# Optimization experiments

Measured on AMD Instinct MI355X. Metric: run time of the kernel, lower is better.

Reference implementation:

```python
import jax, jax.numpy as jnp
import numpy as np

DIM = 1024
N_HEADS = 16
HEAD_DIM = DIM // N_HEADS
BATCH = 2
SEQ = 2048


def rotate_half(x):
    x1, x2 = jnp.split(x, 2, axis=-1)
    return jnp.concatenate((-x2, x1), axis=-1)


def rope_cos_sin(seq_len, head_dim, dtype=jnp.float32):
    inv_freq = 1.0 / (10000.0 ** (jnp.arange(0, head_dim, 2, dtype=jnp.float32) / head_dim))
    t = jnp.arange(seq_len, dtype=jnp.float32)
    freqs = jnp.einsum('i,j->ij', t, inv_freq)          # [S, hd/2]
    emb = jnp.concatenate((freqs, freqs), axis=-1)       # [S, hd]
    return emb.astype(dtype)[None, :, None, :]           # [1, S, 1, hd] (cos/sin applied below)


def setup_inputs() -> dict:
    key = jax.random.key(0)
    k_x, k_q, k_k, k_v, k_o = jax.random.split(key, 5)
    scale = 1.0 / np.sqrt(DIM)
    x = jax.random.normal(k_x, (BATCH, SEQ, DIM), dtype=jnp.float32)
    Wq = jax.random.normal(k_q, (DIM, DIM), dtype=jnp.float32) * scale
    Wk = jax.random.normal(k_k, (DIM, DIM), dtype=jnp.float32) * scale
    Wv = jax.random.normal(k_v, (DIM, DIM), dtype=jnp.float32) * scale
    Wo = jax.random.normal(k_o, (DIM, DIM), dtype=jnp.float32) * scale
    # causal mask: scores masked where mask == 0
    mask = jnp.tril(jnp.ones((SEQ, SEQ), dtype=jnp.int32))[None, None, :, :]
    return {"x": x, "Wq": Wq, "Wk": Wk, "Wv": Wv, "Wo": Wo, "mask": mask}


def reference(x, Wq, Wk, Wv, Wo, mask):
    B, S, _ = x.shape
    # torch nn.Linear: y = x @ W.T
    q = (x @ Wq.T).reshape(B, S, N_HEADS, HEAD_DIM)
    k = (x @ Wk.T).reshape(B, S, N_HEADS, HEAD_DIM)
    v = (x @ Wv.T).reshape(B, S, N_HEADS, HEAD_DIM)
    ang = rope_cos_sin(S, HEAD_DIM, x.dtype)
    cos, sin = jnp.cos(ang), jnp.sin(ang)
    q = q * cos + rotate_half(q) * sin
    k = k * cos + rotate_half(k) * sin
    # [B, H, S, hd]
    q = q.transpose(0, 2, 1, 3)
    k = k.transpose(0, 2, 1, 3)
    v = v.transpose(0, 2, 1, 3)
    scores = jnp.einsum('bhqd,bhkd->bhqk', q, k) / np.sqrt(HEAD_DIM)
    scores = jnp.where(mask == 0, jnp.asarray(-1e9, scores.dtype), scores)
    attn = jax.nn.softmax(scores, axis=-1)
    out = jnp.einsum('bhqk,bhkd->bhqd', attn, v)
    out = out.transpose(0, 2, 1, 3).reshape(B, S, DIM)
    return out @ Wo.T
```

## Files before the change

### kernel.cpp

```cpp
#include <hip/hip_runtime.h>
#include <stdint.h>

typedef unsigned short u16;
typedef __bf16 bf16x8 __attribute__((ext_vector_type(8)));
typedef __bf16 bf16x4 __attribute__((ext_vector_type(4)));
typedef float f32x4 __attribute__((ext_vector_type(4)));

#define N_B 2
#define N_S 2048
#define N_D 1024
#define N_H 16
#define HD 64

#if __has_builtin(__builtin_amdgcn_exp2f)
#define EXP2F(x) __builtin_amdgcn_exp2f(x)
#else
#define EXP2F(x) exp2f(x)
#endif

__device__ __forceinline__ u16 f2bf(float f) {
  union { float f; uint32_t u; } v; v.f = f;
  uint32_t u = v.u + 0x7fffu + ((v.u >> 16) & 1u);
  return (u16)(u >> 16);
}

__device__ __forceinline__ void gload16(const u16* g, u16* lds) {
  __builtin_amdgcn_global_load_lds(
      (const __attribute__((address_space(1))) unsigned int*)g,
      (__attribute__((address_space(3))) unsigned int*)lds, 16, 0, 0);
}

__global__ __launch_bounds__(256) void prep_kernel(
    const float* __restrict__ x, const float* __restrict__ Wq,
    const float* __restrict__ Wk, const float* __restrict__ Wv,
    const float* __restrict__ Wo,
    u16* __restrict__ xb, u16* __restrict__ wqb, u16* __restrict__ wkb,
    u16* __restrict__ wvb, u16* __restrict__ wob,
    float* __restrict__ cosT, float* __restrict__ sinT)
{
  const int NX = N_B * N_S * N_D;
  const int NW = N_D * N_D;
  int bid = blockIdx.x;
  if (bid < 8192) {
    int i = (bid * 256 + threadIdx.x) * 4;
    const float* src; u16* dst; int off;
    if (i < NX) { src = x; dst = xb; off = i; }
    else {
      int j = i - NX;
      int w = j >> 20;
      off = j & (NW - 1);
      src = (w == 0) ? Wq : (w == 1) ? Wk : (w == 2) ? Wv : Wo;
      dst = (w == 0) ? wqb : (w == 1) ? wkb : (w == 2) ? wvb : wob;
    }
    float4 v = *(const float4*)(src + off);
    ushort4 o;
    o.x = f2bf(v.x); o.y = f2bf(v.y); o.z = f2bf(v.z); o.w = f2bf(v.w);
    *(ushort4*)(dst + off) = o;
  } else {
    int t = (bid - 8192) * 256 + threadIdx.x;
    int s = t >> 5, i = t & 31;
    float inv = expf(-(float)i * 0.28782313662425574f);
    float a = (float)s * inv;
    float sn, cs;
    sincosf(a, &sn, &cs);
    cosT[t] = cs;
    sinT[t] = sn;
  }
}

__global__ __launch_bounds__(256, 5) void proj_kernel(
    const u16* __restrict__ x, const u16* __restrict__ Wq,
    const u16* __restrict__ Wk, const u16* __restrict__ Wv,
    u16* __restrict__ Qb, u16* __restrict__ Kb, u16* __restrict__ Vtb,
    const float* __restrict__ cosT, const float* __restrict__ sinT)
{
  const int mode = blockIdx.z;
  const u16* Wm = (mode == 0) ? Wq : (mode == 1) ? Wk : Wv;
  const int bx = blockIdx.x, by = blockIdx.y;
  const int tid = threadIdx.x;
  const int wave = tid >> 6, lane = tid & 63;
  const int c = lane & 15, quad = lane >> 4;

  __shared__ __align__(16) u16 As[128 * 64];
  __shared__ __align__(16) u16 Bs[64 * 64];

  const f32x4 zero = {0.f, 0.f, 0.f, 0.f};
  f32x4 acc[2][4];
#pragma unroll
  for (int i = 0; i < 2; ++i)
#pragma unroll
    for (int j = 0; j < 4; ++j) acc[i][j] = zero;

  for (int kt = 0; kt < 16; ++kt) {
    const int k0 = kt * 64;
    __syncthreads();
#pragma unroll
    for (int t = 0; t < 4; ++t) {
      int p = t * 256 + tid;
      int m = p >> 3, sl = p & 7;
      int kq = sl ^ (m & 7);
      gload16(x + (size_t)(by * 128 + m) * N_D + k0 + kq * 8, &As[(t * 256 + wave * 64) * 8]);
    }
#pragma unroll
    for (int t = 0; t < 2; ++t) {
      int p = t * 256 + tid;
      int m = p >> 3, sl = p & 7;
      int kq = sl ^ (m & 7);
      gload16(Wm + (size_t)(bx * 64 + m) * N_D + k0 + kq * 8, &Bs[(t * 256 + wave * 64) * 8]);
    }
    __syncthreads();
#pragma unroll
    for (int ks = 0; ks < 2; ++ks) {
      bf16x8 av[2], bv[4];
      int kq = ks * 4 + quad;
#pragma unroll
      for (int i = 0; i < 2; ++i) {
        int m = wave * 32 + i * 16 + c;
        av[i] = *(const bf16x8*)&As[(m * 8 + (kq ^ (m & 7))) * 8];
      }
#pragma unroll
      for (int j = 0; j < 4; ++j) {
        int n = j * 16 + c;
        bv[j] = *(const bf16x8*)&Bs[(n * 8 + (kq ^ (n & 7))) * 8];
      }
#pragma unroll
      for (int i = 0; i < 2; ++i)
#pragma unroll
        for (int j = 0; j < 4; ++j)
          acc[i][j] = __builtin_amdgcn_mfma_f32_16x16x32_bf16(av[i], bv[j], acc[i][j], 0, 0, 0);
    }
  }

  const int h = bx;
  if (mode < 2) {
    u16* Out = (mode == 0) ? Qb : Kb;
#pragma unroll
    for (int i = 0; i < 2; ++i) {
#pragma unroll
      for (int r = 0; r < 4; ++r) {
        int row = by * 128 + wave * 32 + i * 16 + quad * 4 + r;
        int b = row >> 11, s = row & 2047;
        float cs0 = cosT[s * 32 + c],      sn0 = sinT[s * 32 + c];
        float cs1 = cosT[s * 32 + 16 + c], sn1 = sinT[s * 32 + 16 + c];
        size_t base = ((size_t)(b * N_H + h) * N_S + s) * HD;
#pragma unroll
        for (int j = 0; j < 4; ++j) {
          float v = acc[i][j][r];
          float p = acc[i][j ^ 2][r];
          float cs = (j & 1) ? cs1 : cs0;
          float sn = (j & 1) ? sn1 : sn0;
          float res = (j < 2) ? (v * cs - p * sn) : (v * cs + p * sn);
          Out[base + j * 16 + c] = f2bf(res);
        }
      }
    }
  } else {
#pragma unroll
    for (int i = 0; i < 2; ++i) {
      int srow = by * 128 + wave * 32 + i * 16 + quad * 4;
      int b = srow >> 11, sb = srow & 2047;
#pragma unroll
      for (int j = 0; j < 4; ++j) {
        int d = j * 16 + c;
        ushort4 pk;
        pk.x = f2bf(acc[i][j][0]);
        pk.y = f2bf(acc[i][j][1]);
        pk.z = f2bf(acc[i][j][2]);
        pk.w = f2bf(acc[i][j][3]);
        *(ushort4*)&Vtb[((size_t)(b * N_H + h) * HD + d) * N_S + sb] = pk;
      }
    }
  }
}

__global__ __launch_bounds__(128, 2) void attn_kernel(
    const u16* __restrict__ Qb, const u16* __restrict__ Kb,
    const u16* __restrict__ Vtb, u16* __restrict__ Ab)
{
  const int tid = threadIdx.x;
  const int wave = tid >> 6;
  const int lane = tid & 63;
  const int c = lane & 15, quad = lane >> 4;
  const int bx = blockIdx.x;
  const int xcd = bx & 7;
  const int idx = bx >> 3;
  const int t = 63 - (idx >> 2);
  const int bh = xcd + (idx & 3) * 8;
  const int q0 = t * 32;
  const int nk = (t >> 1) + 1;
  const int nk0 = (nk + 1) >> 1;
  const int kb0 = wave ? nk0 : 0;
  const int ke = wave ? nk : nk0;
  const int maskch = t & 1;

  __shared__ __align__(16) u16 Ks[2][2][64 * 64];
  __shared__ __align__(16) u16 Ps[2][32 * 32];

  const u16* Qg = Qb + ((size_t)bh * N_S + q0) * HD;
  const u16* Kg = Kb + (size_t)bh * N_S * HD;
  const u16* Vg = Vtb + (size_t)bh * HD * N_S;
  u16* Psw = &Ps[wave][0];
  u16* Ksw = &Ks[wave][0][0];

  bf16x8 qreg[2][2];
#pragma unroll
  for (int jQ = 0; jQ < 2; ++jQ)
#pragma unroll
    for (int ks = 0; ks < 2; ++ks)
      qreg[jQ][ks] = *(const bf16x8*)(Qg + (jQ * 16 + c) * HD + ks * 32 + quad * 8);

  const f32x4 zero = {0.f, 0.f, 0.f, 0.f};
  f32x4 acc_o[2][4];
#pragma unroll
  for (int mt = 0; mt < 2; ++mt)
#pragma unroll
    for (int nt = 0; nt < 4; ++nt) acc_o[mt][nt] = zero;
  float lrow[2] = {0.f, 0.f};

  const float CLOG = 0.18033688011112042f;
  const float FM = 16.0f;

  bf16x8 vf[2][4];

  if (kb0 < ke) {
#pragma unroll
    for (int i = 0; i < 8; ++i) {
      int ci = i * 64 + lane;
      int m = ci >> 3, sl = ci & 7;
      int kq = sl ^ (m & 7);
      gload16(Kg + (size_t)(kb0 * 64 + m) * HD + kq * 8,
              &Ksw[(kb0 & 1) * 4096 + i * 512]);
    }
    asm volatile("" ::: "memory");
#pragma unroll
    for (int ch = 0; ch < 2; ++ch)
#pragma unroll
      for (int nt = 0; nt < 4; ++nt)
        vf[ch][nt] = *(const bf16x8*)(Vg + (size_t)(nt * 16 + c) * N_S
                                      + kb0 * 64 + ch * 32 + quad * 8);
  }

  for (int kt = kb0; kt < ke; ++kt) {
    const u16* kbp = &Ksw[(kt & 1) * 4096];
    if (kt + 1 < ke) {
#pragma unroll
      for (int i = 0; i < 8; ++i) {
        int ci = i * 64 + lane;
        int m = ci >> 3, sl = ci & 7;
        int kq = sl ^ (m & 7);
        gload16(Kg + (size_t)((kt + 1) * 64 + m) * HD + kq * 8,
                &Ksw[((kt + 1) & 1) * 4096 + i * 512]);
      }
      asm volatile("s_waitcnt vmcnt(16)" ::: "memory");
    } else {
      asm volatile("s_waitcnt vmcnt(8)" ::: "memory");
    }

    const bool diag = (kt == nk - 1);
    const int nch = (diag && maskch == 0) ? 1 : 2;

#pragma unroll
    for (int ch = 0; ch < 2; ++ch) {
      if (ch < nch) {
        f32x4 acc_s[2][2];
#pragma unroll
        for (int iK = 0; iK < 2; ++iK)
#pragma unroll
          for (int jQ = 0; jQ < 2; ++jQ) acc_s[iK][jQ] = zero;
#pragma unroll
        for (int ks = 0; ks < 2; ++ks) {
          bf16x8 kf[2];
          int kq = ks * 4 + quad;
#pragma unroll
          for (int iK = 0; iK < 2; ++iK) {
            int m = ch * 32 + iK * 16 + c;
            kf[iK] = *(const bf16x8*)&kbp[(m * 8 + (kq ^ (m & 7))) * 8];
          }
#pragma unroll
          for (int iK = 0; iK < 2; ++iK)
#pragma unroll
            for (int jQ = 0; jQ < 2; ++jQ)
              acc_s[iK][jQ] = __builtin_amdgcn_mfma_f32_16x16x32_bf16(
                  kf[iK], qreg[jQ][ks], acc_s[iK][jQ], 0, 0, 0);
        }

        const bool domask = diag && (ch == maskch);
#pragma unroll
        for (int iK = 0; iK < 2; ++iK)
#pragma unroll
          for (int jQ = 0; jQ < 2; ++jQ) {
            bf16x4 pb;
#pragma unroll
            for (int rr = 0; rr < 4; ++rr) {
              float arg = fmaf(acc_s[iK][jQ][rr], CLOG, -FM);
              if (domask) {
                int dsk = iK * 16 + quad * 4 + rr;
                int dq = jQ * 16 + c;
                if (dsk > dq) arg = -3.0e38f;
              }
              float p = EXP2F(arg);
              lrow[jQ] += p;
              pb[rr] = (__bf16)p;
            }
            int q = jQ * 16 + c;
            int slot = (iK * 2 + (quad >> 1)) ^ (q & 3);
            *(bf16x4*)&Psw[q * 32 + slot * 8 + (quad & 1) * 4] = pb;
          }

        bf16x8 pf[2];
#pragma unroll
        for (int mt = 0; mt < 2; ++mt) {
          int q = mt * 16 + c;
          pf[mt] = *(const bf16x8*)&Psw[q * 32 + ((quad ^ (q & 3)) * 8)];
        }
#pragma unroll
        for (int mt = 0; mt < 2; ++mt)
#pragma unroll
          for (int nt = 0; nt < 4; ++nt)
            acc_o[mt][nt] = __builtin_amdgcn_mfma_f32_16x16x32_bf16(
                pf[mt], vf[ch][nt], acc_o[mt][nt], 0, 0, 0);
      }
    }

    if (kt + 1 < ke) {
#pragma unroll
      for (int ch = 0; ch < 2; ++ch)
#pragma unroll
        for (int nt = 0; nt < 4; ++nt)
          vf[ch][nt] = *(const bf16x8*)(Vg + (size_t)(nt * 16 + c) * N_S
                                        + (kt + 1) * 64 + ch * 32 + quad * 8);
    }
  }

#pragma unroll
  for (int jQ = 0; jQ < 2; ++jQ) {
    float l = lrow[jQ];
    l += __shfl_xor(l, 16, 64);
    l += __shfl_xor(l, 32, 64);
    lrow[jQ] = l;
  }

  float* Osh = (float*)&Ks[1][0][0];
  float* Lsh = Osh + 32 * 65;
  if (wave == 1) {
#pragma unroll
    for (int mt = 0; mt < 2; ++mt)
#pragma unroll
      for (int nt = 0; nt < 4; ++nt)
#pragma unroll
        for (int rr = 0; rr < 4; ++rr)
          Osh[(mt * 16 + quad * 4 + rr) * 65 + nt * 16 + c] = acc_o[mt][nt][rr];
    if (quad == 0) { Lsh[c] = lrow[0]; Lsh[16 + c] = lrow[1]; }
  }
  __syncthreads();
  if (wave == 0) {
    float inv[2];
#pragma unroll
    for (int jQ = 0; jQ < 2; ++jQ)
      inv[jQ] = 1.0f / (lrow[jQ] + Lsh[jQ * 16 + c]);
    const int b = bh >> 4, h = bh & 15;
#pragma unroll
    for (int mt = 0; mt < 2; ++mt) {
#pragma unroll
      for (int rr = 0; rr < 4; ++rr) {
        float iv = __shfl(inv[mt], quad * 4 + rr, 64);
        int lr = mt * 16 + quad * 4 + rr;
        int q = q0 + lr;
#pragma unroll
        for (int nt = 0; nt < 4; ++nt) {
          float val = (acc_o[mt][nt][rr] + Osh[lr * 65 + nt * 16 + c]) * iv;
          Ab[((size_t)(b * N_S + q)) * N_D + h * HD + nt * 16 + c] = f2bf(val);
        }
      }
    }
  }
}

__global__ __launch_bounds__(256) void out_gemm_kernel(
    const u16* __restrict__ A, const u16* __restrict__ Wo, float* __restrict__ out)
{
  const int bx = blockIdx.x, by = blockIdx.y;
  const int tid = threadIdx.x;
  const int wave = tid >> 6, lane = tid & 63;
  const int c = lane & 15, quad = lane >> 4;
  const int wm = wave & 1, wn = wave >> 1;

  __shared__ __align__(16) u16 As[64 * 64];
  __shared__ __align__(16) u16 Bs[64 * 64];

  const f32x4 zero = {0.f, 0.f, 0.f, 0.f};
  f32x4 acc[2][2];
#pragma unroll
  for (int i = 0; i < 2; ++i)
#pragma unroll
    for (int j = 0; j < 2; ++j) acc[i][j] = zero;

  for (int kt = 0; kt < 16; ++kt) {
    const int k0 = kt * 64;
    __syncthreads();
#pragma unroll
    for (int t = 0; t < 2; ++t) {
      int p = t * 256 + tid;
      int m = p >> 3, sl = p & 7;
      int kq = sl ^ (m & 7);
      gload16(A + (size_t)(by * 64 + m) * N_D + k0 + kq * 8, &As[(t * 256 + wave * 64) * 8]);
    }
#pragma unroll
    for (int t = 0; t < 2; ++t) {
      int p = t * 256 + tid;
      int m = p >> 3, sl = p & 7;
      int kq = sl ^ (m & 7);
      gload16(Wo + (size_t)(bx * 64 + m) * N_D + k0 + kq * 8, &Bs[(t * 256 + wave * 64) * 8]);
    }
    __syncthreads();
#pragma unroll
    for (int ks = 0; ks < 2; ++ks) {
      bf16x8 av[2], bv[2];
      int kq = ks * 4 + quad;
#pragma unroll
      for (int i = 0; i < 2; ++i) {
        int m = wm * 32 + i * 16 + c;
        av[i] = *(const bf16x8*)&As[(m * 8 + (kq ^ (m & 7))) * 8];
      }
#pragma unroll
      for (int j = 0; j < 2; ++j) {
        int n = wn * 32 + j * 16 + c;
        bv[j] = *(const bf16x8*)&Bs[(n * 8 + (kq ^ (n & 7))) * 8];
      }
#pragma unroll
      for (int i = 0; i < 2; ++i)
#pragma unroll
        for (int j = 0; j < 2; ++j)
          acc[i][j] = __builtin_amdgcn_mfma_f32_16x16x32_bf16(av[i], bv[j], acc[i][j], 0, 0, 0);
    }
  }

#pragma unroll
  for (int i = 0; i < 2; ++i)
#pragma unroll
    for (int r = 0; r < 4; ++r) {
      int row = by * 64 + wm * 32 + i * 16 + quad * 4 + r;
#pragma unroll
      for (int j = 0; j < 2; ++j) {
        int col = bx * 64 + wn * 32 + j * 16 + c;
        out[(size_t)row * N_D + col] = acc[i][j][r];
      }
    }
}

extern "C" void kernel_launch(void* const* d_in, const int* in_sizes, int n_in,
                              void* d_out, int out_size, void* d_ws, size_t ws_size,
                              hipStream_t stream) {
  const float* x  = (const float*)d_in[0];
  const float* Wq = (const float*)d_in[1];
  const float* Wk = (const float*)d_in[2];
  const float* Wv = (const float*)d_in[3];
  const float* Wo = (const float*)d_in[4];
  float* out = (float*)d_out;
  char* ws = (char*)d_ws;
  u16* xb   = (u16*)(ws);
  u16* Wqb  = (u16*)(ws + ( 8u << 20));
  u16* Wkb  = (u16*)(ws + (10u << 20));
  u16* Wvb  = (u16*)(ws + (12u << 20));
  u16* Wob  = (u16*)(ws + (14u << 20));
  u16* Qb   = (u16*)(ws + (16u << 20));
  u16* Kb   = (u16*)(ws + (24u << 20));
  u16* Vtb  = (u16*)(ws + (32u << 20));
  u16* Ab   = (u16*)(ws + (40u << 20));
  float* cosT = (float*)(ws + (48u << 20));
  float* sinT = (float*)(ws + (48u << 20) + (1u << 20));

  prep_kernel<<<8448, 256, 0, stream>>>(x, Wq, Wk, Wv, Wo,
                                        xb, Wqb, Wkb, Wvb, Wob, cosT, sinT);
  proj_kernel<<<dim3(16, 32, 3), 256, 0, stream>>>(xb, Wqb, Wkb, Wvb, Qb, Kb, Vtb, cosT, sinT);
  attn_kernel<<<2048, 128, 0, stream>>>(Qb, Kb, Vtb, Ab);
  out_gemm_kernel<<<dim3(16, 64), 256, 0, stream>>>(Ab, Wob, out);
}
```

Before: 200.1 us.

## Shrink attention key tile to 32 rows and raise occupancy to four blocks

The attention loop now walks the causal range in 32-key chunks instead of 64-key tiles. This halves the K shared-memory double buffer and the V register fragments, which is what lets launch bounds go from 2 to 4 blocks per SM. The diagonal masking becomes a simple check on the last chunk, so the partial-tile handling goes away, and the two waves split the work at 32-key granularity. In exchange there are twice as many loop iterations, each with its own barrier-free prefetch and wait, and the output staging buffer loses its padding column, which may bring back LDS bank conflicts.

```diff
diff --git a/kernel.cpp b/kernel.cpp
--- a/kernel.cpp
+++ b/kernel.cpp
@@ -173,7 +173,7 @@
   }
 }
 
-__global__ __launch_bounds__(128, 2) void attn_kernel(
+__global__ __launch_bounds__(128, 4) void attn_kernel(
     const u16* __restrict__ Qb, const u16* __restrict__ Kb,
     const u16* __restrict__ Vtb, u16* __restrict__ Ab)
 {
@@ -187,13 +187,12 @@
   const int t = 63 - (idx >> 2);
   const int bh = xcd + (idx & 3) * 8;
   const int q0 = t * 32;
-  const int nk = (t >> 1) + 1;
-  const int nk0 = (nk + 1) >> 1;
-  const int kb0 = wave ? nk0 : 0;
-  const int ke = wave ? nk : nk0;
-  const int maskch = t & 1;
-
-  __shared__ __align__(16) u16 Ks[2][2][64 * 64];
+  const int nc = t + 1;
+  const int nc0 = (nc + 1) >> 1;
+  const int cb = wave ? nc0 : 0;
+  const int ce = wave ? nc : nc0;
+
+  __shared__ __align__(16) u16 Ks[2][2][32 * 64];
   __shared__ __align__(16) u16 Ps[2][32 * 32];
 
   const u16* Qg = Qb + ((size_t)bh * N_S + q0) * HD;
@@ -220,115 +219,104 @@
   const float CLOG = 0.18033688011112042f;
   const float FM = 16.0f;
 
-  bf16x8 vf[2][4];
-
-  if (kb0 < ke) {
-#pragma unroll
-    for (int i = 0; i < 8; ++i) {
+  bf16x8 vf[4];
+
+  if (cb < ce) {
+#pragma unroll
+    for (int i = 0; i < 4; ++i) {
       int ci = i * 64 + lane;
       int m = ci >> 3, sl = ci & 7;
       int kq = sl ^ (m & 7);
-      gload16(Kg + (size_t)(kb0 * 64 + m) * HD + kq * 8,
-              &Ksw[(kb0 & 1) * 4096 + i * 512]);
+      gload16(Kg + (size_t)(cb * 32 + m) * HD + kq * 8,
+              &Ksw[(cb & 1) * 2048 + i * 512]);
     }
     asm volatile("" ::: "memory");
 #pragma unroll
-    for (int ch = 0; ch < 2; ++ch)
-#pragma unroll
-      for (int nt = 0; nt < 4; ++nt)
-        vf[ch][nt] = *(const bf16x8*)(Vg + (size_t)(nt * 16 + c) * N_S
-                                      + kb0 * 64 + ch * 32 + quad * 8);
-  }
-
-  for (int kt = kb0; kt < ke; ++kt) {
-    const u16* kbp = &Ksw[(kt & 1) * 4096];
-    if (kt + 1 < ke) {
-#pragma unroll
-      for (int i = 0; i < 8; ++i) {
+    for (int nt = 0; nt < 4; ++nt)
+      vf[nt] = *(const bf16x8*)(Vg + (size_t)(nt * 16 + c) * N_S
+                                + cb * 32 + quad * 8);
+  }
+
+  for (int cc = cb; cc < ce; ++cc) {
+    const u16* kbp = &Ksw[(cc & 1) * 2048];
+    if (cc + 1 < ce) {
+#pragma unroll
+      for (int i = 0; i < 4; ++i) {
         int ci = i * 64 + lane;
         int m = ci >> 3, sl = ci & 7;
         int kq = sl ^ (m & 7);
-        gload16(Kg + (size_t)((kt + 1) * 64 + m) * HD + kq * 8,
-                &Ksw[((kt + 1) & 1) * 4096 + i * 512]);
-      }
-      asm volatile("s_waitcnt vmcnt(16)" ::: "memory");
+        gload16(Kg + (size_t)((cc + 1) * 32 + m) * HD + kq * 8,
+                &Ksw[((cc + 1) & 1) * 2048 + i * 512]);
+      }
+      asm volatile("s_waitcnt vmcnt(8)" ::: "memory");
     } else {
-      asm volatile("s_waitcnt vmcnt(8)" ::: "memory");
-    }
-
-    const bool diag = (kt == nk - 1);
-    const int nch = (diag && maskch == 0) ? 1 : 2;
-
-#pragma unroll
-    for (int ch = 0; ch < 2; ++ch) {
-      if (ch < nch) {
-        f32x4 acc_s[2][2];
-#pragma unroll
-        for (int iK = 0; iK < 2; ++iK)
-#pragma unroll
-          for (int jQ = 0; jQ < 2; ++jQ) acc_s[iK][jQ] = zero;
-#pragma unroll
-        for (int ks = 0; ks < 2; ++ks) {
-          bf16x8 kf[2];
-          int kq = ks * 4 + quad;
-#pragma unroll
-          for (int iK = 0; iK < 2; ++iK) {
-            int m = ch * 32 + iK * 16 + c;
-            kf[iK] = *(const bf16x8*)&kbp[(m * 8 + (kq ^ (m & 7))) * 8];
+      asm volatile("s_waitcnt vmcnt(4)" ::: "memory");
+    }
+
+    const bool domask = (cc == t);
+
+    f32x4 acc_s[2][2];
+#pragma unroll
+    for (int iK = 0; iK < 2; ++iK)
+#pragma unroll
+      for (int jQ = 0; jQ < 2; ++jQ) acc_s[iK][jQ] = zero;
+#pragma unroll
+    for (int ks = 0; ks < 2; ++ks) {
+      bf16x8 kf[2];
+      int kq = ks * 4 + quad;
+#pragma unroll
+      for (int iK = 0; iK < 2; ++iK) {
+        int m = iK * 16 + c;
+        kf[iK] = *(const bf16x8*)&kbp[(m * 8 + (kq ^ (m & 7))) * 8];
+      }
+#pragma unroll
+      for (int iK = 0; iK < 2; ++iK)
+#pragma unroll
+        for (int jQ = 0; jQ < 2; ++jQ)
+          acc_s[iK][jQ] = __builtin_amdgcn_mfma_f32_16x16x32_bf16(
+              kf[iK], qreg[jQ][ks], acc_s[iK][jQ], 0, 0, 0);
+    }
+
+#pragma unroll
+    for (int iK = 0; iK < 2; ++iK)
+#pragma unroll
+      for (int jQ = 0; jQ < 2; ++jQ) {
+        bf16x4 pb;
+#pragma unroll
+        for (int rr = 0; rr < 4; ++rr) {
+          float arg = fmaf(acc_s[iK][jQ][rr], CLOG, -FM);
+          if (domask) {
+            int dsk = iK * 16 + quad * 4 + rr;
+            int dq = jQ * 16 + c;
+            if (dsk > dq) arg = -3.0e38f;
           }
-#pragma unroll
-          for (int iK = 0; iK < 2; ++iK)
-#pragma unroll
-            for (int jQ = 0; jQ < 2; ++jQ)
-              acc_s[iK][jQ] = __builtin_amdgcn_mfma_f32_16x16x32_bf16(
-                  kf[iK], qreg[jQ][ks], acc_s[iK][jQ], 0, 0, 0);
+          float p = EXP2F(arg);
+          lrow[jQ] += p;
+          pb[rr] = (__bf16)p;
         }
-
-        const bool domask = diag && (ch == maskch);
-#pragma unroll
-        for (int iK = 0; iK < 2; ++iK)
-#pragma unroll
-          for (int jQ = 0; jQ < 2; ++jQ) {
-            bf16x4 pb;
-#pragma unroll
-            for (int rr = 0; rr < 4; ++rr) {
-              float arg = fmaf(acc_s[iK][jQ][rr], CLOG, -FM);
-              if (domask) {
-                int dsk = iK * 16 + quad * 4 + rr;
-                int dq = jQ * 16 + c;
-                if (dsk > dq) arg = -3.0e38f;
-              }
-              float p = EXP2F(arg);
-              lrow[jQ] += p;
-              pb[rr] = (__bf16)p;
-            }
-            int q = jQ * 16 + c;
-            int slot = (iK * 2 + (quad >> 1)) ^ (q & 3);
-            *(bf16x4*)&Psw[q * 32 + slot * 8 + (quad & 1) * 4] = pb;
-          }
-
-        bf16x8 pf[2];
-#pragma unroll
-        for (int mt = 0; mt < 2; ++mt) {
-          int q = mt * 16 + c;
-          pf[mt] = *(const bf16x8*)&Psw[q * 32 + ((quad ^ (q & 3)) * 8)];
-        }
-#pragma unroll
-        for (int mt = 0; mt < 2; ++mt)
-#pragma unroll
-          for (int nt = 0; nt < 4; ++nt)
-            acc_o[mt][nt] = __builtin_amdgcn_mfma_f32_16x16x32_bf16(
-                pf[mt], vf[ch][nt], acc_o[mt][nt], 0, 0, 0);
-      }
-    }
-
-    if (kt + 1 < ke) {
-#pragma unroll
-      for (int ch = 0; ch < 2; ++ch)
-#pragma unroll
-        for (int nt = 0; nt < 4; ++nt)
-          vf[ch][nt] = *(const bf16x8*)(Vg + (size_t)(nt * 16 + c) * N_S
-                                        + (kt + 1) * 64 + ch * 32 + quad * 8);
+        int q = jQ * 16 + c;
+        int slot = (iK * 2 + (quad >> 1)) ^ (q & 3);
+        *(bf16x4*)&Psw[q * 32 + slot * 8 + (quad & 1) * 4] = pb;
+      }
+
+    bf16x8 pf[2];
+#pragma unroll
+    for (int mt = 0; mt < 2; ++mt) {
+      int q = mt * 16 + c;
+      pf[mt] = *(const bf16x8*)&Psw[q * 32 + ((quad ^ (q & 3)) * 8)];
+    }
+#pragma unroll
+    for (int mt = 0; mt < 2; ++mt)
+#pragma unroll
+      for (int nt = 0; nt < 4; ++nt)
+        acc_o[mt][nt] = __builtin_amdgcn_mfma_f32_16x16x32_bf16(
+            pf[mt], vf[nt], acc_o[mt][nt], 0, 0, 0);
+
+    if (cc + 1 < ce) {
+#pragma unroll
+      for (int nt = 0; nt < 4; ++nt)
+        vf[nt] = *(const bf16x8*)(Vg + (size_t)(nt * 16 + c) * N_S
+                                  + (cc + 1) * 32 + quad * 8);
     }
   }
 
@@ -341,7 +329,7 @@
   }
 
   float* Osh = (float*)&Ks[1][0][0];
-  float* Lsh = Osh + 32 * 65;
+  float* Lsh = (float*)&Ps[1][0];
   if (wave == 1) {
 #pragma unroll
     for (int mt = 0; mt < 2; ++mt)
@@ -349,7 +337,7 @@
       for (int nt = 0; nt < 4; ++nt)
 #pragma unroll
         for (int rr = 0; rr < 4; ++rr)
-          Osh[(mt * 16 + quad * 4 + rr) * 65 + nt * 16 + c] = acc_o[mt][nt][rr];
+          Osh[(mt * 16 + quad * 4 + rr) * 64 + nt * 16 + c] = acc_o[mt][nt][rr];
     if (quad == 0) { Lsh[c] = lrow[0]; Lsh[16 + c] = lrow[1]; }
   }
   __syncthreads();
@@ -368,7 +356,7 @@
         int q = q0 + lr;
 #pragma unroll
         for (int nt = 0; nt < 4; ++nt) {
-          float val = (acc_o[mt][nt][rr] + Osh[lr * 65 + nt * 16 + c]) * iv;
+          float val = (acc_o[mt][nt][rr] + Osh[lr * 64 + nt * 16 + c]) * iv;
           Ab[((size_t)(b * N_S + q)) * N_D + h * HD + nt * 16 + c] = f2bf(val);
         }
       }
```

Result: no change. 196.7 us (-1.7%).

## Share K tile staging across two query-tile waves in 4-wave attention blocks

Applied to the files above, without the earlier changes.

The attention kernel moves from 2-wave blocks covering one 32-row query tile to 4-wave blocks covering two adjacent query tiles. Each pair of waves shares the key range split. Both query waves cooperatively load the same K tile into shared memory, halving redundant K global traffic, with a block barrier each iteration to coordinate the double buffer. This adds barrier synchronisation and some idle iterations for waves with fewer key blocks.

```diff
diff --git a/kernel.cpp b/kernel.cpp
--- a/kernel.cpp
+++ b/kernel.cpp
@@ -173,7 +173,7 @@
   }
 }
 
-__global__ __launch_bounds__(128, 2) void attn_kernel(
+__global__ __launch_bounds__(256, 4) void attn_kernel(
     const u16* __restrict__ Qb, const u16* __restrict__ Kb,
     const u16* __restrict__ Vtb, u16* __restrict__ Ab)
 {
@@ -181,26 +181,26 @@
   const int wave = tid >> 6;
   const int lane = tid & 63;
   const int c = lane & 15, quad = lane >> 4;
+  const int kw = wave >> 1, qw = wave & 1;
   const int bx = blockIdx.x;
   const int xcd = bx & 7;
-  const int idx = bx >> 3;
-  const int t = 63 - (idx >> 2);
-  const int bh = xcd + (idx & 3) * 8;
-  const int q0 = t * 32;
-  const int nk = (t >> 1) + 1;
-  const int nk0 = (nk + 1) >> 1;
-  const int kb0 = wave ? nk0 : 0;
-  const int ke = wave ? nk : nk0;
-  const int maskch = t & 1;
-
-  __shared__ __align__(16) u16 Ks[2][2][64 * 64];
-  __shared__ __align__(16) u16 Ps[2][32 * 32];
+  const int i0 = bx >> 3;
+  const int T = 31 - (i0 >> 2);
+  const int bh = xcd + (i0 & 3) * 8;
+  const int q0 = (2 * T + qw) * 32;
+  const int nk = T + 1;
+  const int h0 = (nk + 1) >> 1;
+  const int h1 = nk - h0;
+  const int my_n = kw ? h1 : h0;
+  const int jbase = kw ? h0 : 0;
+
+  __shared__ __align__(16) u16 Kbuf[2][2][64 * 64];
+  __shared__ __align__(16) u16 Ps[4][1024];
 
   const u16* Qg = Qb + ((size_t)bh * N_S + q0) * HD;
   const u16* Kg = Kb + (size_t)bh * N_S * HD;
   const u16* Vg = Vtb + (size_t)bh * HD * N_S;
   u16* Psw = &Ps[wave][0];
-  u16* Ksw = &Ks[wave][0][0];
 
   bf16x8 qreg[2][2];
 #pragma unroll
@@ -222,115 +222,116 @@
 
   bf16x8 vf[2][4];
 
-  if (kb0 < ke) {
-#pragma unroll
-    for (int i = 0; i < 8; ++i) {
-      int ci = i * 64 + lane;
-      int m = ci >> 3, sl = ci & 7;
-      int kq = sl ^ (m & 7);
-      gload16(Kg + (size_t)(kb0 * 64 + m) * HD + kq * 8,
-              &Ksw[(kb0 & 1) * 4096 + i * 512]);
-    }
+#define STAGEK(j_, buf_)                                                      \
+  {                                                                           \
+    _Pragma("unroll") for (int t2 = 0; t2 < 4; ++t2) {                        \
+      int p = t2 * 128 + qw * 64 + lane;                                      \
+      int m = p >> 3, sl = p & 7;                                             \
+      int kq = sl ^ (m & 7);                                                  \
+      gload16(Kg + (size_t)((j_) * 64 + m) * HD + kq * 8,                     \
+              &Kbuf[kw][buf_][(t2 * 128 + qw * 64) * 8]);                     \
+    }                                                                         \
+  }
+
+  if (0 < my_n) {
+    STAGEK(jbase, 0);
     asm volatile("" ::: "memory");
 #pragma unroll
     for (int ch = 0; ch < 2; ++ch)
 #pragma unroll
       for (int nt = 0; nt < 4; ++nt)
         vf[ch][nt] = *(const bf16x8*)(Vg + (size_t)(nt * 16 + c) * N_S
-                                      + kb0 * 64 + ch * 32 + quad * 8);
-  }
-
-  for (int kt = kb0; kt < ke; ++kt) {
-    const u16* kbp = &Ksw[(kt & 1) * 4096];
-    if (kt + 1 < ke) {
-#pragma unroll
-      for (int i = 0; i < 8; ++i) {
-        int ci = i * 64 + lane;
-        int m = ci >> 3, sl = ci & 7;
-        int kq = sl ^ (m & 7);
-        gload16(Kg + (size_t)((kt + 1) * 64 + m) * HD + kq * 8,
-                &Ksw[((kt + 1) & 1) * 4096 + i * 512]);
-      }
-      asm volatile("s_waitcnt vmcnt(16)" ::: "memory");
-    } else {
-      asm volatile("s_waitcnt vmcnt(8)" ::: "memory");
-    }
-
-    const bool diag = (kt == nk - 1);
-    const int nch = (diag && maskch == 0) ? 1 : 2;
-
-#pragma unroll
-    for (int ch = 0; ch < 2; ++ch) {
-      if (ch < nch) {
-        f32x4 acc_s[2][2];
-#pragma unroll
-        for (int iK = 0; iK < 2; ++iK)
-#pragma unroll
-          for (int jQ = 0; jQ < 2; ++jQ) acc_s[iK][jQ] = zero;
-#pragma unroll
-        for (int ks = 0; ks < 2; ++ks) {
-          bf16x8 kf[2];
-          int kq = ks * 4 + quad;
-#pragma unroll
-          for (int iK = 0; iK < 2; ++iK) {
-            int m = ch * 32 + iK * 16 + c;
-            kf[iK] = *(const bf16x8*)&kbp[(m * 8 + (kq ^ (m & 7))) * 8];
+                                      + jbase * 64 + ch * 32 + quad * 8);
+  }
+
+  for (int it = 0; it < h0; ++it) {
+    const int j = jbase + it;
+    const bool have = it < my_n;
+    asm volatile("s_waitcnt vmcnt(8)" ::: "memory");
+    __builtin_amdgcn_s_barrier();
+    __builtin_amdgcn_sched_barrier(0);
+
+    if (it + 1 < my_n) STAGEK(j + 1, (it + 1) & 1);
+
+    if (have) {
+      const u16* kbp = &Kbuf[kw][it & 1][0];
+      const bool diag = (j == T);
+      const int nch = (diag && qw == 0) ? 1 : 2;
+
+#pragma unroll
+      for (int ch = 0; ch < 2; ++ch) {
+        if (ch < nch) {
+          f32x4 acc_s[2][2];
+#pragma unroll
+          for (int iK = 0; iK < 2; ++iK)
+#pragma unroll
+            for (int jQ = 0; jQ < 2; ++jQ) acc_s[iK][jQ] = zero;
+#pragma unroll
+          for (int ks = 0; ks < 2; ++ks) {
+            bf16x8 kf[2];
+            int kq = ks * 4 + quad;
+#pragma unroll
+            for (int iK = 0; iK < 2; ++iK) {
+              int m = ch * 32 + iK * 16 + c;
+              kf[iK] = *(const bf16x8*)&kbp[(m * 8 + (kq ^ (m & 7))) * 8];
+            }
+#pragma unroll
+            for (int iK = 0; iK < 2; ++iK)
+#pragma unroll
+              for (int jQ = 0; jQ < 2; ++jQ)
+                acc_s[iK][jQ] = __builtin_amdgcn_mfma_f32_16x16x32_bf16(
+                    kf[iK], qreg[jQ][ks], acc_s[iK][jQ], 0, 0, 0);
           }
+
+          const bool domask = diag && (ch == qw);
 #pragma unroll
           for (int iK = 0; iK < 2; ++iK)
 #pragma unroll
-            for (int jQ = 0; jQ < 2; ++jQ)
-              acc_s[iK][jQ] = __builtin_amdgcn_mfma_f32_16x16x32_bf16(
-                  kf[iK], qreg[jQ][ks], acc_s[iK][jQ], 0, 0, 0);
+            for (int jQ = 0; jQ < 2; ++jQ) {
+              bf16x4 pb;
+#pragma unroll
+              for (int rr = 0; rr < 4; ++rr) {
+                float arg = fmaf(acc_s[iK][jQ][rr], CLOG, -FM);
+                if (domask) {
+                  int dsk = iK * 16 + quad * 4 + rr;
+                  int dq = jQ * 16 + c;
+                  if (dsk > dq) arg = -3.0e38f;
+                }
+                float p = EXP2F(arg);
+                lrow[jQ] += p;
+                pb[rr] = (__bf16)p;
+              }
+              int q = jQ * 16 + c;
+              int slot = (iK * 2 + (quad >> 1)) ^ (q & 3);
+              *(bf16x4*)&Psw[q * 32 + slot * 8 + (quad & 1) * 4] = pb;
+            }
+
+          bf16x8 pf[2];
+#pragma unroll
+          for (int mt = 0; mt < 2; ++mt) {
+            int q = mt * 16 + c;
+            pf[mt] = *(const bf16x8*)&Psw[q * 32 + ((quad ^ (q & 3)) * 8)];
+          }
+#pragma unroll
+          for (int mt = 0; mt < 2; ++mt)
+#pragma unroll
+            for (int nt = 0; nt < 4; ++nt)
+              acc_o[mt][nt] = __builtin_amdgcn_mfma_f32_16x16x32_bf16(
+                  pf[mt], vf[ch][nt], acc_o[mt][nt], 0, 0, 0);
         }
-
-        const bool domask = diag && (ch == maskch);
-#pragma unroll
-        for (int iK = 0; iK < 2; ++iK)
-#pragma unroll
-          for (int jQ = 0; jQ < 2; ++jQ) {
-            bf16x4 pb;
-#pragma unroll
-            for (int rr = 0; rr < 4; ++rr) {
-              float arg = fmaf(acc_s[iK][jQ][rr], CLOG, -FM);
-              if (domask) {
-                int dsk = iK * 16 + quad * 4 + rr;
-                int dq = jQ * 16 + c;
-                if (dsk > dq) arg = -3.0e38f;
-              }
-              float p = EXP2F(arg);
-              lrow[jQ] += p;
-              pb[rr] = (__bf16)p;
-            }
-            int q = jQ * 16 + c;
-            int slot = (iK * 2 + (quad >> 1)) ^ (q & 3);
-            *(bf16x4*)&Psw[q * 32 + slot * 8 + (quad & 1) * 4] = pb;
-          }
-
-        bf16x8 pf[2];
-#pragma unroll
-        for (int mt = 0; mt < 2; ++mt) {
-          int q = mt * 16 + c;
-          pf[mt] = *(const bf16x8*)&Psw[q * 32 + ((quad ^ (q & 3)) * 8)];
-        }
-#pragma unroll
-        for (int mt = 0; mt < 2; ++mt)
+      }
+
+      if (it + 1 < my_n) {
+#pragma unroll
+        for (int ch = 0; ch < 2; ++ch)
 #pragma unroll
           for (int nt = 0; nt < 4; ++nt)
-            acc_o[mt][nt] = __builtin_amdgcn_mfma_f32_16x16x32_bf16(
-                pf[mt], vf[ch][nt], acc_o[mt][nt], 0, 0, 0);
-      }
-    }
-
-    if (kt + 1 < ke) {
-#pragma unroll
-      for (int ch = 0; ch < 2; ++ch)
-#pragma unroll
-        for (int nt = 0; nt < 4; ++nt)
-          vf[ch][nt] = *(const bf16x8*)(Vg + (size_t)(nt * 16 + c) * N_S
-                                        + (kt + 1) * 64 + ch * 32 + quad * 8);
-    }
-  }
+            vf[ch][nt] = *(const bf16x8*)(Vg + (size_t)(nt * 16 + c) * N_S
+                                          + (j + 1) * 64 + ch * 32 + quad * 8);
+      }
+    }
+  }
+#undef STAGEK
 
 #pragma unroll
   for (int jQ = 0; jQ < 2; ++jQ) {
@@ -340,24 +341,29 @@
     lrow[jQ] = l;
   }
 
-  float* Osh = (float*)&Ks[1][0][0];
-  float* Lsh = Osh + 32 * 65;
-  if (wave == 1) {
+  __syncthreads();
+  float* Osc = (float*)&Kbuf[0][0][0];
+  float* myO = Osc + qw * 32 * 65;
+  if (kw == 1) {
 #pragma unroll
     for (int mt = 0; mt < 2; ++mt)
 #pragma unroll
       for (int nt = 0; nt < 4; ++nt)
 #pragma unroll
-        for (int rr = 0; rr < 4; ++rr)
-          Osh[(mt * 16 + quad * 4 + rr) * 65 + nt * 16 + c] = acc_o[mt][nt][rr];
-    if (quad == 0) { Lsh[c] = lrow[0]; Lsh[16 + c] = lrow[1]; }
+        for (int r = 0; r < 4; ++r)
+          myO[(mt * 16 + quad * 4 + r) * 65 + nt * 16 + c] = acc_o[mt][nt][r];
+    if (quad == 0) {
+      float* Lw = (float*)&Ps[wave][0];
+      Lw[c] = lrow[0]; Lw[16 + c] = lrow[1];
+    }
   }
   __syncthreads();
-  if (wave == 0) {
+  if (kw == 0) {
+    const float* pl = (const float*)&Ps[wave + 2][0];
     float inv[2];
 #pragma unroll
     for (int jQ = 0; jQ < 2; ++jQ)
-      inv[jQ] = 1.0f / (lrow[jQ] + Lsh[jQ * 16 + c]);
+      inv[jQ] = 1.0f / (lrow[jQ] + pl[jQ * 16 + c]);
     const int b = bh >> 4, h = bh & 15;
 #pragma unroll
     for (int mt = 0; mt < 2; ++mt) {
@@ -368,7 +374,7 @@
         int q = q0 + lr;
 #pragma unroll
         for (int nt = 0; nt < 4; ++nt) {
-          float val = (acc_o[mt][nt][rr] + Osh[lr * 65 + nt * 16 + c]) * iv;
+          float val = (acc_o[mt][nt][rr] + myO[lr * 65 + nt * 16 + c]) * iv;
           Ab[((size_t)(b * N_S + q)) * N_D + h * HD + nt * 16 + c] = f2bf(val);
         }
       }
@@ -473,6 +479,6 @@
   prep_kernel<<<8448, 256, 0, stream>>>(x, Wq, Wk, Wv, Wo,
                                         xb, Wqb, Wkb, Wvb, Wob, cosT, sinT);
   proj_kernel<<<dim3(16, 32, 3), 256, 0, stream>>>(xb, Wqb, Wkb, Wvb, Qb, Kb, Vtb, cosT, sinT);
-  attn_kernel<<<2048, 128, 0, stream>>>(Qb, Kb, Vtb, Ab);
+  attn_kernel<<<1024, 256, 0, stream>>>(Qb, Kb, Vtb, Ab);
   out_gemm_kernel<<<dim3(16, 64), 256, 0, stream>>>(Ab, Wob, out);
 }
```

Result: slower. 229.4 us (+14.6%).

## Restructure projection GEMMs with per-wave double-buffered A and register-direct B loads

Applied to the files above, without the earlier changes.

Both the QKV projection and output GEMM now give each wave a private double-buffered LDS tile for its 32 rows of A. The next tile is prefetched asynchronously and synchronised with s_waitcnt instead of block-wide __syncthreads. B (weight) fragments are loaded straight from global memory into registers, and the block index is remapped so that blocks sharing a weight column tile land on the same XCD for L2 reuse. The output GEMM tile grows to 128x64, halving its grid. The cost is more register pressure, reliance on hand-counted vmcnt values, and uncoalesced direct global B reads.

```diff
diff --git a/kernel.cpp b/kernel.cpp
--- a/kernel.cpp
+++ b/kernel.cpp
@@ -68,21 +68,40 @@
   }
 }
 
-__global__ __launch_bounds__(256, 5) void proj_kernel(
+__global__ __launch_bounds__(256) void proj_kernel(
     const u16* __restrict__ x, const u16* __restrict__ Wq,
     const u16* __restrict__ Wk, const u16* __restrict__ Wv,
     u16* __restrict__ Qb, u16* __restrict__ Kb, u16* __restrict__ Vtb,
     const float* __restrict__ cosT, const float* __restrict__ sinT)
 {
-  const int mode = blockIdx.z;
-  const u16* Wm = (mode == 0) ? Wq : (mode == 1) ? Wk : Wv;
-  const int bx = blockIdx.x, by = blockIdx.y;
   const int tid = threadIdx.x;
   const int wave = tid >> 6, lane = tid & 63;
   const int c = lane & 15, quad = lane >> 4;
-
-  __shared__ __align__(16) u16 As[128 * 64];
-  __shared__ __align__(16) u16 Bs[64 * 64];
+  const int bid = blockIdx.x;
+  const int xcd = bid & 7;
+  const int g = bid >> 3;
+  const int band = xcd + 8 * (g & 3);
+  const int a2 = g >> 2;
+  const int bx = a2 & 15;
+  const int mode = a2 >> 4;
+  const u16* Wm = (mode == 0) ? Wq : (mode == 1) ? Wk : Wv;
+  const int row0 = band * 128 + wave * 32;
+
+  __shared__ __align__(16) u16 Asw[4][2][32 * 64];
+
+  const u16* Ag = x + (size_t)row0 * N_D;
+  u16* Aw = &Asw[wave][0][0];
+
+#define STAGEA(kt_, buf_)                                                     \
+  {                                                                           \
+    _Pragma("unroll") for (int i = 0; i < 4; ++i) {                           \
+      int ci = i * 64 + lane;                                                 \
+      int m = ci >> 3, sl = ci & 7;                                           \
+      int kq = sl ^ (m & 7);                                                  \
+      gload16(Ag + (size_t)m * N_D + (kt_) * 64 + kq * 8,                     \
+              &Aw[(buf_) * 2048 + i * 512]);                                  \
+    }                                                                         \
+  }
 
   const f32x4 zero = {0.f, 0.f, 0.f, 0.f};
   f32x4 acc[2][4];
@@ -91,45 +110,53 @@
 #pragma unroll
     for (int j = 0; j < 4; ++j) acc[i][j] = zero;
 
+  bf16x8 bvf[2][4];
+
+  STAGEA(0, 0);
+  asm volatile("" ::: "memory");
+#pragma unroll
+  for (int ks = 0; ks < 2; ++ks)
+#pragma unroll
+    for (int j = 0; j < 4; ++j)
+      bvf[ks][j] = *(const bf16x8*)(Wm + (size_t)(bx * 64 + j * 16 + c) * N_D
+                                    + ks * 32 + quad * 8);
+
   for (int kt = 0; kt < 16; ++kt) {
-    const int k0 = kt * 64;
-    __syncthreads();
-#pragma unroll
-    for (int t = 0; t < 4; ++t) {
-      int p = t * 256 + tid;
-      int m = p >> 3, sl = p & 7;
-      int kq = sl ^ (m & 7);
-      gload16(x + (size_t)(by * 128 + m) * N_D + k0 + kq * 8, &As[(t * 256 + wave * 64) * 8]);
-    }
-#pragma unroll
-    for (int t = 0; t < 2; ++t) {
-      int p = t * 256 + tid;
-      int m = p >> 3, sl = p & 7;
-      int kq = sl ^ (m & 7);
-      gload16(Wm + (size_t)(bx * 64 + m) * N_D + k0 + kq * 8, &Bs[(t * 256 + wave * 64) * 8]);
-    }
-    __syncthreads();
+    const u16* ab = &Aw[(kt & 1) * 2048];
+    if (kt + 1 < 16) {
+      STAGEA(kt + 1, (kt + 1) & 1);
+      asm volatile("s_waitcnt vmcnt(12)" ::: "memory");
+    } else {
+      asm volatile("s_waitcnt vmcnt(8)" ::: "memory");
+    }
+
 #pragma unroll
     for (int ks = 0; ks < 2; ++ks) {
-      bf16x8 av[2], bv[4];
+      bf16x8 av[2];
       int kq = ks * 4 + quad;
 #pragma unroll
       for (int i = 0; i < 2; ++i) {
-        int m = wave * 32 + i * 16 + c;
-        av[i] = *(const bf16x8*)&As[(m * 8 + (kq ^ (m & 7))) * 8];
-      }
-#pragma unroll
-      for (int j = 0; j < 4; ++j) {
-        int n = j * 16 + c;
-        bv[j] = *(const bf16x8*)&Bs[(n * 8 + (kq ^ (n & 7))) * 8];
+        int m = i * 16 + c;
+        av[i] = *(const bf16x8*)&ab[(m * 8 + (kq ^ (m & 7))) * 8];
       }
 #pragma unroll
       for (int i = 0; i < 2; ++i)
 #pragma unroll
         for (int j = 0; j < 4; ++j)
-          acc[i][j] = __builtin_amdgcn_mfma_f32_16x16x32_bf16(av[i], bv[j], acc[i][j], 0, 0, 0);
-    }
-  }
+          acc[i][j] = __builtin_amdgcn_mfma_f32_16x16x32_bf16(
+              av[i], bvf[ks][j], acc[i][j], 0, 0, 0);
+    }
+
+    if (kt + 1 < 16) {
+#pragma unroll
+      for (int ks = 0; ks < 2; ++ks)
+#pragma unroll
+        for (int j = 0; j < 4; ++j)
+          bvf[ks][j] = *(const bf16x8*)(Wm + (size_t)(bx * 64 + j * 16 + c) * N_D
+                                        + (kt + 1) * 64 + ks * 32 + quad * 8);
+    }
+  }
+#undef STAGEA
 
   const int h = bx;
   if (mode < 2) {
@@ -138,7 +165,7 @@
     for (int i = 0; i < 2; ++i) {
 #pragma unroll
       for (int r = 0; r < 4; ++r) {
-        int row = by * 128 + wave * 32 + i * 16 + quad * 4 + r;
+        int row = row0 + i * 16 + quad * 4 + r;
         int b = row >> 11, s = row & 2047;
         float cs0 = cosT[s * 32 + c],      sn0 = sinT[s * 32 + c];
         float cs1 = cosT[s * 32 + 16 + c], sn1 = sinT[s * 32 + 16 + c];
@@ -157,7 +184,7 @@
   } else {
 #pragma unroll
     for (int i = 0; i < 2; ++i) {
-      int srow = by * 128 + wave * 32 + i * 16 + quad * 4;
+      int srow = row0 + i * 16 + quad * 4;
       int b = srow >> 11, sb = srow & 2047;
 #pragma unroll
       for (int j = 0; j < 4; ++j) {
@@ -379,70 +406,95 @@
 __global__ __launch_bounds__(256) void out_gemm_kernel(
     const u16* __restrict__ A, const u16* __restrict__ Wo, float* __restrict__ out)
 {
-  const int bx = blockIdx.x, by = blockIdx.y;
   const int tid = threadIdx.x;
   const int wave = tid >> 6, lane = tid & 63;
   const int c = lane & 15, quad = lane >> 4;
-  const int wm = wave & 1, wn = wave >> 1;
-
-  __shared__ __align__(16) u16 As[64 * 64];
-  __shared__ __align__(16) u16 Bs[64 * 64];
+  const int bid = blockIdx.x;
+  const int xcd = bid & 7;
+  const int g = bid >> 3;
+  const int band = xcd + 8 * (g & 3);
+  const int bx = g >> 2;
+  const int row0 = band * 128 + wave * 32;
+
+  __shared__ __align__(16) u16 Asw[4][2][32 * 64];
+
+  const u16* Ag = A + (size_t)row0 * N_D;
+  u16* Aw = &Asw[wave][0][0];
+
+#define STAGEA(kt_, buf_)                                                     \
+  {                                                                           \
+    _Pragma("unroll") for (int i = 0; i < 4; ++i) {                           \
+      int ci = i * 64 + lane;                                                 \
+      int m = ci >> 3, sl = ci & 7;                                           \
+      int kq = sl ^ (m & 7);                                                  \
+      gload16(Ag + (size_t)m * N_D + (kt_) * 64 + kq * 8,                     \
+              &Aw[(buf_) * 2048 + i * 512]);                                  \
+    }                                                                         \
+  }
 
   const f32x4 zero = {0.f, 0.f, 0.f, 0.f};
-  f32x4 acc[2][2];
+  f32x4 acc[2][4];
 #pragma unroll
   for (int i = 0; i < 2; ++i)
 #pragma unroll
-    for (int j = 0; j < 2; ++j) acc[i][j] = zero;
+    for (int j = 0; j < 4; ++j) acc[i][j] = zero;
+
+  bf16x8 bvf[2][4];
+
+  STAGEA(0, 0);
+  asm volatile("" ::: "memory");
+#pragma unroll
+  for (int ks = 0; ks < 2; ++ks)
+#pragma unroll
+    for (int j = 0; j < 4; ++j)
+      bvf[ks][j] = *(const bf16x8*)(Wo + (size_t)(bx * 64 + j * 16 + c) * N_D
+                                    + ks * 32 + quad * 8);
 
   for (int kt = 0; kt < 16; ++kt) {
-    const int k0 = kt * 64;
-    __syncthreads();
-#pragma unroll
-    for (int t = 0; t < 2; ++t) {
-      int p = t * 256 + tid;
-      int m = p >> 3, sl = p & 7;
-      int kq = sl ^ (m & 7);
-      gload16(A + (size_t)(by * 64 + m) * N_D + k0 + kq * 8, &As[(t * 256 + wave * 64) * 8]);
-    }
-#pragma unroll
-    for (int t = 0; t < 2; ++t) {
-      int p = t * 256 + tid;
-      int m = p >> 3, sl = p & 7;
-      int kq = sl ^ (m & 7);
-      gload16(Wo + (size_t)(bx * 64 + m) * N_D + k0 + kq * 8, &Bs[(t * 256 + wave * 64) * 8]);
-    }
-    __syncthreads();
+    const u16* ab = &Aw[(kt & 1) * 2048];
+    if (kt + 1 < 16) {
+      STAGEA(kt + 1, (kt + 1) & 1);
+      asm volatile("s_waitcnt vmcnt(12)" ::: "memory");
+    } else {
+      asm volatile("s_waitcnt vmcnt(8)" ::: "memory");
+    }
+
 #pragma unroll
     for (int ks = 0; ks < 2; ++ks) {
-      bf16x8 av[2], bv[2];
+      bf16x8 av[2];
       int kq = ks * 4 + quad;
 #pragma unroll
       for (int i = 0; i < 2; ++i) {
-        int m = wm * 32 + i * 16 + c;
-        av[i] = *(const bf16x8*)&As[(m * 8 + (kq ^ (m & 7))) * 8];
-      }
-#pragma unroll
-      for (int j = 0; j < 2; ++j) {
-        int n = wn * 32 + j * 16 + c;
-        bv[j] = *(const bf16x8*)&Bs[(n * 8 + (kq ^ (n & 7))) * 8];
+        int m = i * 16 + c;
+        av[i] = *(const bf16x8*)&ab[(m * 8 + (kq ^ (m & 7))) * 8];
       }
 #pragma unroll
       for (int i = 0; i < 2; ++i)
 #pragma unroll
-        for (int j = 0; j < 2; ++j)
-          acc[i][j] = __builtin_amdgcn_mfma_f32_16x16x32_bf16(av[i], bv[j], acc[i][j], 0, 0, 0);
-    }
-  }
+        for (int j = 0; j < 4; ++j)
+          acc[i][j] = __builtin_amdgcn_mfma_f32_16x16x32_bf16(
+              av[i], bvf[ks][j], acc[i][j], 0, 0, 0);
+    }
+
+    if (kt + 1 < 16) {
+#pragma unroll
+      for (int ks = 0; ks < 2; ++ks)
+#pragma unroll
+        for (int j = 0; j < 4; ++j)
+          bvf[ks][j] = *(const bf16x8*)(Wo + (size_t)(bx * 64 + j * 16 + c) * N_D
+                                        + (kt + 1) * 64 + ks * 32 + quad * 8);
+    }
+  }
+#undef STAGEA
 
 #pragma unroll
   for (int i = 0; i < 2; ++i)
 #pragma unroll
     for (int r = 0; r < 4; ++r) {
-      int row = by * 64 + wm * 32 + i * 16 + quad * 4 + r;
-#pragma unroll
-      for (int j = 0; j < 2; ++j) {
-        int col = bx * 64 + wn * 32 + j * 16 + c;
+      int row = row0 + i * 16 + quad * 4 + r;
+#pragma unroll
+      for (int j = 0; j < 4; ++j) {
+        int col = bx * 64 + j * 16 + c;
         out[(size_t)row * N_D + col] = acc[i][j][r];
       }
     }
@@ -472,7 +524,7 @@
 
   prep_kernel<<<8448, 256, 0, stream>>>(x, Wq, Wk, Wv, Wo,
                                         xb, Wqb, Wkb, Wvb, Wob, cosT, sinT);
-  proj_kernel<<<dim3(16, 32, 3), 256, 0, stream>>>(xb, Wqb, Wkb, Wvb, Qb, Kb, Vtb, cosT, sinT);
+  proj_kernel<<<1536, 256, 0, stream>>>(xb, Wqb, Wkb, Wvb, Qb, Kb, Vtb, cosT, sinT);
   attn_kernel<<<2048, 128, 0, stream>>>(Qb, Kb, Vtb, Ab);
-  out_gemm_kernel<<<dim3(16, 64), 256, 0, stream>>>(Ab, Wob, out);
-}
+  out_gemm_kernel<<<512, 256, 0, stream>>>(Ab, Wob, out);
+}
```

After: 275.1 us. +37.5%, slower.
